# Kernel optimization log

Hardware: AMD Instinct MI355X
Metric: run time of the kernel (lower is better)

The kernel has to match this reference:

```python
import jax, jax.numpy as jnp
import numpy as np

LAM_S = 0.7
LAM_L = 0.3
ANCHOR_PAGES = 4
FLOW_WINDOW = 8
FLASH_TOP_K = 32
Q_MAX = 32
NEG = -10000.0


def setup_inputs() -> dict:
    B, N, P, Dp = 8, 1024, 64, 1024
    L = N * P
    key = jax.random.key(0)
    ks = jax.random.split(key, 9)
    block_repr = jax.random.normal(ks[0], (B, N, Dp), jnp.float32)
    query_hidden = jax.random.normal(ks[1], (B, Dp), jnp.float32)
    input_ids = jax.random.randint(ks[2], (B, L), 0, 32000, jnp.int32)
    token_level_weights = jax.random.uniform(ks[3], (B, L), jnp.float32)
    token_valid = jnp.ones((B, L), bool)
    page_valid = jax.random.uniform(ks[4], (B, N, P)) < 0.97
    page_indices = jnp.broadcast_to(jnp.arange(L, dtype=jnp.int32).reshape(1, N, P), (B, N, P))
    token2page = jnp.broadcast_to((jnp.arange(L, dtype=jnp.int32) // P)[None, :], (B, L))
    segment_ids = jax.random.randint(ks[5], (B, N), 0, 4, jnp.int32)
    query_pos = jax.random.randint(ks[6], (B,), L // 2, L, jnp.int32)
    query_start = jax.random.randint(ks[7], (B,), 0, L - Q_MAX, jnp.int32)
    query_end = query_start + jax.random.randint(ks[8], (B,), 0, Q_MAX, jnp.int32)
    return dict(block_repr=block_repr, query_hidden=query_hidden, query_pos=query_pos,
                input_ids=input_ids, token_level_weights=token_level_weights,
                query_start=query_start, query_end=query_end, segment_ids=segment_ids,
                page_valid=page_valid, page_indices=page_indices,
                token2page=token2page, token_valid=token_valid)


def _l2norm(x):
    # F.normalize: x / max(||x||, eps)
    return x / jnp.maximum(jnp.linalg.norm(x, axis=-1, keepdims=True), 1e-12)


def _norm_scores(scores, mask):
    # per-batch min-max normalization over masked entries, 0 elsewhere
    v_min = jnp.where(mask, scores, jnp.inf).min(axis=1, keepdims=True)
    v_max = jnp.where(mask, scores, -jnp.inf).max(axis=1, keepdims=True)
    rng = v_max - v_min
    flat = rng < 1e-6  # includes empty-mask rows (rng = -inf)
    normed = jnp.where(flat, 0.0, (scores - v_min) / jnp.where(flat, 1.0, rng))
    return jnp.where(mask, normed, 0.0)


def reference(block_repr, query_hidden, query_pos, input_ids, token_level_weights,
              query_start, query_end, segment_ids, page_valid, page_indices,
              token2page, token_valid):
    B, N, Dp = block_repr.shape
    L = input_ids.shape[1]
    P = page_valid.shape[2]

    # ---- semantic scores (single query vector path) ----
    k_vec = _l2norm(block_repr)                       # [B,N,Dp]
    q_vec = _l2norm(query_hidden)                     # [B,Dp]
    scores_sem = jnp.einsum('bd,bnd->bn', q_vec, k_vec)

    # ---- lexical scores ----
    qs = jnp.clip(query_start, 0, L - 1)
    qe = jnp.clip(query_end, 0, L - 1)
    j = jnp.arange(Q_MAX, dtype=jnp.int32)
    pos = jnp.clip(qs[:, None] + j[None, :], 0, L - 1)            # [B,Q]
    qmask = (j[None, :] <= (qe - qs)[:, None]) & (query_end >= query_start)[:, None]
    qmask = qmask & jnp.take_along_axis(token_valid, pos, axis=1)
    q_ids = jnp.where(qmask, jnp.take_along_axis(input_ids, pos, axis=1), -1)  # [B,Q], -1 never matches

    idx_flat = page_indices.reshape(B, N * P)
    tok = jnp.take_along_axis(input_ids, idx_flat, axis=1).reshape(B, N, P)
    w_page = jnp.take_along_axis(token_level_weights, idx_flat, axis=1).reshape(B, N, P)
    in_q = (tok[..., None] == q_ids[:, None, None, :]).any(-1)    # [B,N,P] isin
    scores_lex = jnp.where(page_valid & in_q, w_page, 0.0).sum(-1)  # [B,N]

    # ---- masks ----
    query_page = jnp.clip(jnp.take_along_axis(token2page, query_pos[:, None], axis=1)[:, 0], 0)
    page_idx = jnp.arange(N, dtype=jnp.int32)[None, :]
    valid_mask = page_valid.any(-1) & (segment_ids >= 0) & (page_idx <= query_page[:, None])

    sem_n = _norm_scores(scores_sem, valid_mask)
    lex_n = _norm_scores(scores_lex, valid_mask)
    scores_mix = (LAM_S * sem_n + LAM_L * lex_n) / (LAM_S + LAM_L)
    scores_final = jnp.where(valid_mask, scores_mix, NEG)

    # ---- keep-page selection ----
    is_seg0 = (segment_ids == 0) & valid_mask
    anchor = is_seg0 & (jnp.cumsum(is_seg0, axis=1) <= ANCHOR_PAGES)
    lower = jnp.clip(query_page - FLOW_WINDOW, 0)
    flow = (page_idx >= lower[:, None]) & (page_idx <= query_page[:, None]) & valid_mask
    flow = flow.at[jnp.arange(B), query_page].set(True)
    base_keep = anchor | flow
    candidate = valid_mask & ~base_keep
    scores_candidate = jnp.where(candidate, scores_final, NEG)
    k = min(FLASH_TOP_K, N)
    _, topk_idx = jax.lax.top_k(scores_candidate, k)
    flash = jnp.zeros_like(candidate).at[jnp.arange(B)[:, None], topk_idx].set(True) & candidate
    return base_keep | flash
```

## Files before the change

### kernel.cpp

```cpp
#include <hip/hip_runtime.h>
#include <hip/hip_bf16.h>
#include <cstdint>
#include <cstddef>

#define LAM_S_F 0.7f
#define LAM_L_F 0.3f
#define ANCHOR_PAGES 4
#define FLOW_WINDOW 8
#define FLASH_TOP_K 32
#define QMAX 32
#define NEGF (-10000.0f)

__device__ __forceinline__ float wave_sum(float v) {
#pragma unroll
  for (int off = 32; off > 0; off >>= 1) v += __shfl_xor(v, off);
  return v;
}

__global__ __launch_bounds__(256) void qp_scores_kernel(
    const float* __restrict__ block_repr,
    const float* __restrict__ query_hidden,
    const int*   __restrict__ input_ids,
    const float* __restrict__ tok_w,
    const int*   __restrict__ query_start,
    const int*   __restrict__ query_end,
    const int*   __restrict__ page_valid,
    const int*   __restrict__ page_indices,
    const int*   __restrict__ token_valid,
    const int*   __restrict__ token2page,
    const int*   __restrict__ query_pos,
    float* __restrict__ o_sem,
    float* __restrict__ o_lex,
    int*   __restrict__ o_pany,
    int N, int P, int Dp, int L)
{
  const int n   = blockIdx.x;
  const int b   = blockIdx.y;
  const int tid = threadIdx.x;

  const int qp = max(token2page[(size_t)b * L + (size_t)query_pos[b]], 0);
  if (n > qp) {
    if (tid == 0) {
      const size_t o = (size_t)b * N + n;
      o_sem[o] = 0.f; o_lex[o] = 0.f; o_pany[o] = 0;
    }
    return;
  }

  __shared__ int   qids[QMAX];
  __shared__ float part[4][3];

  if (tid < QMAX) {
    const int qsr = query_start[b], qer = query_end[b];
    const int qs = min(max(qsr, 0), L - 1);
    const int qe = min(max(qer, 0), L - 1);
    const int pos = min(qs + tid, L - 1);
    const bool m = (tid <= qe - qs) && (qer >= qsr) &&
                   (token_valid[(size_t)b * L + pos] != 0);
    qids[tid] = m ? input_ids[(size_t)b * L + pos] : -1;
  }

  const float4 kv =
      reinterpret_cast<const float4*>(block_repr + ((size_t)b * N + n) * Dp)[tid];
  const float4 qv =
      reinterpret_cast<const float4*>(query_hidden + (size_t)b * Dp)[tid];
  float s_qk = kv.x * qv.x + kv.y * qv.y + kv.z * qv.z + kv.w * qv.w;
  float s_kk = kv.x * kv.x + kv.y * kv.y + kv.z * kv.z + kv.w * kv.w;
  float s_qq = qv.x * qv.x + qv.y * qv.y + qv.z * qv.z + qv.w * qv.w;

  __syncthreads();

  float lex = 0.f;
  bool  pv  = false;
  if (tid < P) {
    const size_t pbase = ((size_t)b * N + n) * (size_t)P + tid;
    const int   idx = page_indices[pbase];
    pv              = (page_valid[pbase] != 0);
    const int   tk  = input_ids[(size_t)b * L + idx];
    const float w   = tok_w[(size_t)b * L + idx];
    bool match = false;
#pragma unroll
    for (int q = 0; q < QMAX; ++q) match = match || (tk == qids[q]);
    lex = (pv && match) ? w : 0.f;
  }

  s_qk = wave_sum(s_qk);
  s_kk = wave_sum(s_kk);
  s_qq = wave_sum(s_qq);
  const int lane = tid & 63, wid = tid >> 6;
  if (lane == 0) { part[wid][0] = s_qk; part[wid][1] = s_kk; part[wid][2] = s_qq; }

  float lexs = 0.f;
  unsigned long long anyv = 0ull;
  if (wid == 0) {
    lexs = wave_sum(lex);
    anyv = __ballot(pv);
  }
  __syncthreads();

  if (tid == 0) {
    const float S1 = part[0][0] + part[1][0] + part[2][0] + part[3][0];
    const float S2 = part[0][1] + part[1][1] + part[2][1] + part[3][1];
    const float S3 = part[0][2] + part[1][2] + part[2][2] + part[3][2];
    const float sem =
        S1 / (fmaxf(sqrtf(S3), 1e-12f) * fmaxf(sqrtf(S2), 1e-12f));
    const size_t o = (size_t)b * N + n;
    o_sem[o]  = sem;
    o_lex[o]  = lexs;
    o_pany[o] = (anyv != 0ull) ? 1 : 0;
  }
}

__global__ __launch_bounds__(1024) void qp_select_kernel(
    const float* __restrict__ o_sem,
    const float* __restrict__ o_lex,
    const int*   __restrict__ o_pany,
    const int*   __restrict__ segment_ids,
    const int*   __restrict__ token2page,
    const int*   __restrict__ query_pos,
    int* __restrict__ out,
    int N, int L)
{
  const int b    = blockIdx.x;
  const int n    = threadIdx.x;
  const int lane = n & 63;
  const int wid  = n >> 6;
  const int NW   = blockDim.x >> 6;

  __shared__ unsigned long long key_arr[1024];
  __shared__ unsigned char fl_arr[1024];
  __shared__ float wred[16][4];
  __shared__ int   wcnt[16];
  __shared__ float g[4];

  const int qp = max(token2page[(size_t)b * L + (size_t)query_pos[b]], 0);
  const size_t o = (size_t)b * N + n;
  const float sem = o_sem[o];
  const float lex = o_lex[o];
  const int   seg = segment_ids[o];
  const bool  valid = (o_pany[o] != 0) && (seg >= 0) && (n <= qp);

  float smin = valid ? sem : INFINITY;
  float smax = valid ? sem : -INFINITY;
  float lmin = valid ? lex : INFINITY;
  float lmax = valid ? lex : -INFINITY;
#pragma unroll
  for (int off = 32; off > 0; off >>= 1) {
    smin = fminf(smin, __shfl_xor(smin, off));
    smax = fmaxf(smax, __shfl_xor(smax, off));
    lmin = fminf(lmin, __shfl_xor(lmin, off));
    lmax = fmaxf(lmax, __shfl_xor(lmax, off));
  }

  const bool is0 = (seg == 0) && valid;
  const unsigned long long bal = __ballot(is0);
  const int excl = (int)__popcll(bal & ((1ull << lane) - 1ull));

  if (lane == 0) {
    wred[wid][0] = smin; wred[wid][1] = smax;
    wred[wid][2] = lmin; wred[wid][3] = lmax;
    wcnt[wid] = (int)__popcll(bal);
  }
  __syncthreads();

  if (n == 0) {
    float a = INFINITY, bmx = -INFINITY, c = INFINITY, d = -INFINITY;
    for (int w = 0; w < NW; ++w) {
      a   = fminf(a, wred[w][0]);
      bmx = fmaxf(bmx, wred[w][1]);
      c   = fminf(c, wred[w][2]);
      d   = fmaxf(d, wred[w][3]);
    }
    g[0] = a; g[1] = bmx; g[2] = c; g[3] = d;
  }
  int prior = 0;
  for (int w = 0; w < wid; ++w) prior += wcnt[w];
  __syncthreads();

  const int  cum    = prior + excl + (is0 ? 1 : 0);
  const bool anchor = is0 && (cum <= ANCHOR_PAGES);

  const float rng_s = g[1] - g[0];
  const float rng_l = g[3] - g[2];
  const float sem_n = (rng_s < 1e-6f) ? 0.f : (sem - g[0]) / rng_s;
  const float lex_n = (rng_l < 1e-6f) ? 0.f : (lex - g[2]) / rng_l;
  const float mix = (LAM_S_F * sem_n + LAM_L_F * lex_n) / (LAM_S_F + LAM_L_F);

  const int  lower = max(qp - FLOW_WINDOW, 0);
  const bool flow  = ((n >= lower) && (n <= qp) && valid) || (n == qp);
  const bool base_keep = anchor || flow;
  const bool cand = valid && !base_keep;

  const unsigned int sb = __float_as_uint(mix);
  key_arr[n] = cand
      ? ((((unsigned long long)(sb + 1u)) << 10) | (unsigned long long)(1023 - n))
      : 0ull;
  fl_arr[n] = 0;
  __syncthreads();

  if (wid == 0) {
    unsigned long long kk[16];
#pragma unroll
    for (int i = 0; i < 16; ++i) kk[i] = key_arr[lane + (i << 6)];
    for (int t = 0; t < FLASH_TOP_K; ++t) {
      unsigned long long lm = 0ull;
#pragma unroll
      for (int i = 0; i < 16; ++i) lm = (kk[i] > lm) ? kk[i] : lm;
#pragma unroll
      for (int off = 1; off < 64; off <<= 1) {
        const unsigned long long ov = __shfl_xor(lm, off);
        lm = (ov > lm) ? ov : lm;
      }
      if (lm == 0ull) break;
      const int win = 1023 - (int)(lm & 1023ull);
      if ((win & 63) == lane) {
        fl_arr[win] = 1;
#pragma unroll
        for (int i = 0; i < 16; ++i) if (i == (win >> 6)) kk[i] = 0ull;
      }
    }
  }
  __syncthreads();

  out[o] = (base_keep || (fl_arr[n] != 0)) ? 1 : 0;
}

extern "C" void kernel_launch(void* const* d_in, const int* in_sizes, int n_in,
                              void* d_out, int out_size, void* d_ws, size_t ws_size,
                              hipStream_t stream) {
  const float* block_repr   = (const float*)d_in[0];
  const float* query_hidden = (const float*)d_in[1];
  const int*   query_pos    = (const int*)d_in[2];
  const int*   input_ids    = (const int*)d_in[3];
  const float* tok_w        = (const float*)d_in[4];
  const int*   query_start  = (const int*)d_in[5];
  const int*   query_end    = (const int*)d_in[6];
  const int*   segment_ids  = (const int*)d_in[7];
  const int*   page_valid   = (const int*)d_in[8];
  const int*   page_indices = (const int*)d_in[9];
  const int*   token2page   = (const int*)d_in[10];
  const int*   token_valid  = (const int*)d_in[11];

  const int B  = in_sizes[2];
  const int Dp = in_sizes[1] / B;
  const int L  = in_sizes[3] / B;
  const int N  = in_sizes[7] / B;
  const int P  = in_sizes[8] / (B * N);

  float* o_sem  = (float*)d_ws;
  float* o_lex  = o_sem + (size_t)B * N;
  int*   o_pany = (int*)(o_lex + (size_t)B * N);
  int*   out    = (int*)d_out;

  dim3 g1(N, B);
  qp_scores_kernel<<<g1, dim3(256), 0, stream>>>(
      block_repr, query_hidden, input_ids, tok_w, query_start, query_end,
      page_valid, page_indices, token_valid, token2page, query_pos,
      o_sem, o_lex, o_pany, N, P, Dp, L);

  qp_select_kernel<<<dim3(B), dim3(N), 0, stream>>>(
      o_sem, o_lex, o_pany, segment_ids, token2page, query_pos, out, N, L);
}
```

Before: 125.7 us.

## Map one wavefront per page in scores kernel instead of one block per page

Each 256-thread block now handles four pages, one per 64-lane wavefront, with each lane loading four float4s of the page vector. The per-block shared-memory partial reduction and second barrier go away, and the grid shrinks fourfold. This is meant to cut block launch and sync overhead and to give each thread more independent loads in flight. The cost is that wavefronts for pages past the query page still sit in the block until the remaining barrier, and per-lane memory accesses are now strided by four float4s.

```diff
diff --git a/kernel.cpp b/kernel.cpp
--- a/kernel.cpp
+++ b/kernel.cpp
@@ -34,21 +34,16 @@
     int*   __restrict__ o_pany,
     int N, int P, int Dp, int L)
 {
-  const int n   = blockIdx.x;
-  const int b   = blockIdx.y;
-  const int tid = threadIdx.x;
+  const int tid  = threadIdx.x;
+  const int lane = tid & 63;
+  const int wid  = tid >> 6;
+  const int b    = blockIdx.y;
+  const int n    = (blockIdx.x << 2) | wid;
+
+  __shared__ int qids[QMAX];
 
   const int qp = max(token2page[(size_t)b * L + (size_t)query_pos[b]], 0);
-  if (n > qp) {
-    if (tid == 0) {
-      const size_t o = (size_t)b * N + n;
-      o_sem[o] = 0.f; o_lex[o] = 0.f; o_pany[o] = 0;
-    }
-    return;
-  }
-
-  __shared__ int   qids[QMAX];
-  __shared__ float part[4][3];
+  const bool active = (n < N) && (n <= qp);
 
   if (tid < QMAX) {
     const int qsr = query_start[b], qer = query_end[b];
@@ -60,20 +55,36 @@
     qids[tid] = m ? input_ids[(size_t)b * L + pos] : -1;
   }
 
-  const float4 kv =
-      reinterpret_cast<const float4*>(block_repr + ((size_t)b * N + n) * Dp)[tid];
-  const float4 qv =
-      reinterpret_cast<const float4*>(query_hidden + (size_t)b * Dp)[tid];
-  float s_qk = kv.x * qv.x + kv.y * qv.y + kv.z * qv.z + kv.w * qv.w;
-  float s_kk = kv.x * kv.x + kv.y * kv.y + kv.z * kv.z + kv.w * kv.w;
-  float s_qq = qv.x * qv.x + qv.y * qv.y + qv.z * qv.z + qv.w * qv.w;
-
-  __syncthreads();
+  float s_qk = 0.f, s_kk = 0.f, s_qq = 0.f;
+  if (active) {
+    const float4* kb =
+        reinterpret_cast<const float4*>(block_repr + ((size_t)b * N + n) * Dp);
+    const float4* qb =
+        reinterpret_cast<const float4*>(query_hidden + (size_t)b * Dp);
+#pragma unroll
+    for (int i = 0; i < 4; ++i) {
+      const float4 kv = kb[(lane << 2) + i];
+      const float4 qv = qb[(lane << 2) + i];
+      s_qk += kv.x * qv.x + kv.y * qv.y + kv.z * qv.z + kv.w * qv.w;
+      s_kk += kv.x * kv.x + kv.y * kv.y + kv.z * kv.z + kv.w * kv.w;
+      s_qq += qv.x * qv.x + qv.y * qv.y + qv.z * qv.z + qv.w * qv.w;
+    }
+  }
+
+  __syncthreads();
+
+  if (!active) {
+    if (n < N && lane == 0) {
+      const size_t o = (size_t)b * N + n;
+      o_sem[o] = 0.f; o_lex[o] = 0.f; o_pany[o] = 0;
+    }
+    return;
+  }
 
   float lex = 0.f;
   bool  pv  = false;
-  if (tid < P) {
-    const size_t pbase = ((size_t)b * N + n) * (size_t)P + tid;
+  if (lane < P) {
+    const size_t pbase = ((size_t)b * N + n) * (size_t)P + lane;
     const int   idx = page_indices[pbase];
     pv              = (page_valid[pbase] != 0);
     const int   tk  = input_ids[(size_t)b * L + idx];
@@ -87,23 +98,12 @@
   s_qk = wave_sum(s_qk);
   s_kk = wave_sum(s_kk);
   s_qq = wave_sum(s_qq);
-  const int lane = tid & 63, wid = tid >> 6;
-  if (lane == 0) { part[wid][0] = s_qk; part[wid][1] = s_kk; part[wid][2] = s_qq; }
-
-  float lexs = 0.f;
-  unsigned long long anyv = 0ull;
-  if (wid == 0) {
-    lexs = wave_sum(lex);
-    anyv = __ballot(pv);
-  }
-  __syncthreads();
-
-  if (tid == 0) {
-    const float S1 = part[0][0] + part[1][0] + part[2][0] + part[3][0];
-    const float S2 = part[0][1] + part[1][1] + part[2][1] + part[3][1];
-    const float S3 = part[0][2] + part[1][2] + part[2][2] + part[3][2];
+  const float lexs = wave_sum(lex);
+  const unsigned long long anyv = __ballot(pv);
+
+  if (lane == 0) {
     const float sem =
-        S1 / (fmaxf(sqrtf(S3), 1e-12f) * fmaxf(sqrtf(S2), 1e-12f));
+        s_qk / (fmaxf(sqrtf(s_qq), 1e-12f) * fmaxf(sqrtf(s_kk), 1e-12f));
     const size_t o = (size_t)b * N + n;
     o_sem[o]  = sem;
     o_lex[o]  = lexs;
@@ -252,7 +252,7 @@
   int*   o_pany = (int*)(o_lex + (size_t)B * N);
   int*   out    = (int*)d_out;
 
-  dim3 g1(N, B);
+  dim3 g1((N + 3) / 4, B);
   qp_scores_kernel<<<g1, dim3(256), 0, stream>>>(
       block_repr, query_hidden, input_ids, tok_w, query_start, query_end,
       page_valid, page_indices, token_valid, token2page, query_pos,
```

Result: no change. 123.4 us (-1.8%).
